# Optimization experiments

Hardware: AMD Instinct MI355X
Metric: run time of the kernel (lower is better)

The kernel has to match this reference:

```python
import jax, jax.numpy as jnp
import numpy as np

TAU = 2.0  # aggregator_temp


def setup_inputs() -> dict:
    key = jax.random.key(0)
    k1, k2 = jax.random.split(key)
    B, Na, Nv, D = 32, 512, 256, 384
    audio_feats = jax.random.normal(k1, (B, Na, D), dtype=jnp.float32)
    visual_feats = jax.random.normal(k2, (B, Nv, D), dtype=jnp.float32)
    return {"audio_feats": audio_feats, "visual_feats": visual_feats}


def reference(audio_feats, visual_feats):
    # Cross-batch token similarities: (B, B, Na, Nv)
    # token_sims[i, j, n, m] = <audio_feats[i, n], visual_feats[j, m]>
    token_sims = jnp.einsum('ind,jmd->ijnm', audio_feats, visual_feats)
    # logsumexp_pool: tau * logsumexp(sims / tau) over key-token dim (Nv),
    # then mean over query-token dim (Na) -> clip_sims (B, B)
    aggregator = TAU * jax.nn.logsumexp(token_sims / TAU, axis=-1)
    clip_sims = aggregator.mean(axis=-1)
    return clip_sims
```

## Files before the change

### kernel.cpp

```cpp
#include <hip/hip_runtime.h>

constexpr int B_  = 32;
constexpr int Na  = 512;
constexpr int Nv  = 256;
constexpr int D   = 384;

constexpr int NK2 = D / 64;

constexpr int AGROUPS = B_ * 16;
constexpr int BGROUPS = B_ * 8;
constexpr size_t GROUP_BYTES = 12 * 1024;
constexpr int SCALE_ONE = 0x7F7F7F7F;

typedef int   int4v    __attribute__((ext_vector_type(4)));
typedef int   int8v    __attribute__((ext_vector_type(8)));
typedef float floatx16 __attribute__((ext_vector_type(16)));

__device__ __forceinline__ void async_load16(const void* g, void* l) {
    __builtin_amdgcn_global_load_lds(
        (const __attribute__((address_space(1))) unsigned int*)g,
        (__attribute__((address_space(3))) unsigned int*)l,
        16, 0, 0);
}

__global__ void convert_fp8_kernel(const float* __restrict__ a, const float* __restrict__ v,
                                   unsigned char* __restrict__ a8,
                                   unsigned char* __restrict__ b8,
                                   float* __restrict__ out) {
    int gid = blockIdx.x * blockDim.x + threadIdx.x;
    if (gid < B_ * B_) out[gid] = 0.0f;

    const int blk = blockIdx.x / 3;
    const int p   = blockIdx.x % 3;
    const bool isA = blk < AGROUPS;
    const float* src;
    unsigned char* dst;
    if (isA) {
        src = a + (size_t)blk * 32 * D;
        dst = a8 + (size_t)blk * GROUP_BYTES;
    } else {
        int b2 = blk - AGROUPS;
        src = v + (size_t)b2 * 32 * D;
        dst = b8 + (size_t)b2 * GROUP_BYTES;
    }
    const int t = threadIdx.x;
    const int r = t >> 3, q = t & 7;

    int k0 = p * 128 + q * 16;
    const float4* s4 = (const float4*)(src + (size_t)r * D + k0);
    float4 f0 = s4[0], f1 = s4[1], f2 = s4[2], f3 = s4[3];
    int w0 = 0, w1 = 0, w2 = 0, w3 = 0;
    w0 = __builtin_amdgcn_cvt_pk_fp8_f32(f0.x, f0.y, w0, false);
    w0 = __builtin_amdgcn_cvt_pk_fp8_f32(f0.z, f0.w, w0, true);
    w1 = __builtin_amdgcn_cvt_pk_fp8_f32(f1.x, f1.y, w1, false);
    w1 = __builtin_amdgcn_cvt_pk_fp8_f32(f1.z, f1.w, w1, true);
    w2 = __builtin_amdgcn_cvt_pk_fp8_f32(f2.x, f2.y, w2, false);
    w2 = __builtin_amdgcn_cvt_pk_fp8_f32(f2.z, f2.w, w2, true);
    w3 = __builtin_amdgcn_cvt_pk_fp8_f32(f3.x, f3.y, w3, false);
    w3 = __builtin_amdgcn_cvt_pk_fp8_f32(f3.z, f3.w, w3, true);
    int kc = k0 >> 5;
    int h2 = (k0 >> 4) & 1;
    size_t off;
    if (isA) {
        off = (size_t)kc * 1024 + h2 * 512 + r * 16;
    } else {
        int q2 = kc >> 1, u = kc & 1, l = r + 32 * h2;
        off = (size_t)q2 * 2048 + l * 32 + u * 16;
    }
    int4v o = { w0, w1, w2, w3 };
    *(int4v*)(dst + off) = o;
}

__device__ __forceinline__ float expsum16(floatx16 a) {
    constexpr float INV_TAU_LN2 = 0.7213475204444817f;
    float e[16];
    #pragma unroll
    for (int i = 0; i < 16; ++i)
        e[i] = __builtin_amdgcn_exp2f(a[i] * INV_TAU_LN2);
    float t0 = (e[0] + e[1])  + (e[2] + e[3]);
    float t1 = (e[4] + e[5])  + (e[6] + e[7]);
    float t2 = (e[8] + e[9])  + (e[10] + e[11]);
    float t3 = (e[12] + e[13]) + (e[14] + e[15]);
    return (t0 + t1) + (t2 + t3);
}

__global__ __launch_bounds__(256, 2) void gemm_lse_kernel(
        const unsigned char* __restrict__ a8,
        const unsigned char* __restrict__ b8,
        float* __restrict__ out)
{
    __shared__ unsigned char ldsA[48 * 1024];
    __shared__ float ms[4][4][32];

    const int tid  = threadIdx.x;
    const int lane = tid & 63;
    const int wn   = tid >> 6;

    int b = blockIdx.x;
    const int xcd   = b & 7;      b >>= 3;
    const int bi_lo = b & 3;      b >>= 2;
    const int rb    = b & 3;      b >>= 2;
    const int bj    = b;
    const int bi    = xcd * 4 + bi_lo;

    {
        const unsigned char* gsrc = a8 + (size_t)(bi * 16 + rb * 4 + wn) * GROUP_BYTES
                                       + (size_t)lane * 16;
        unsigned char* ldst = ldsA + (size_t)wn * GROUP_BYTES;
        #pragma unroll
        for (int kc = 0; kc < 12; ++kc)
            async_load16(gsrc + (size_t)kc * 1024, ldst + kc * 1024);
    }
    __syncthreads();

    const unsigned char* pv0 = b8 + (size_t)(bj * 8 + wn * 2) * GROUP_BYTES
                                  + (size_t)lane * 32;
    const unsigned char* pv1 = pv0 + GROUP_BYTES;
    const unsigned char* la  = ldsA + (size_t)lane * 16;

    floatx16 acc[4][2];
    #pragma unroll
    for (int g = 0; g < 4; ++g)
        #pragma unroll
        for (int vg = 0; vg < 2; ++vg)
            acc[g][vg] = (floatx16)(0.0f);

    int8v Vc0 = *(const int8v*)pv0;
    int8v Vc1 = *(const int8v*)pv1;

    #pragma unroll
    for (int q2 = 0; q2 < NK2; ++q2) {
        int8v Vn0, Vn1;
        if (q2 + 1 < NK2) {
            Vn0 = *(const int8v*)(pv0 + (size_t)(q2 + 1) * 2048);
            Vn1 = *(const int8v*)(pv1 + (size_t)(q2 + 1) * 2048);
        }
        int8v A[4];
        #pragma unroll
        for (int g = 0; g < 4; ++g) {
            const unsigned char* p = la + (size_t)g * GROUP_BYTES + (size_t)q2 * 2048;
            int4v lo = *(const int4v*)p;
            int4v hi = *(const int4v*)(p + 1024);
            A[g] = __builtin_shufflevector(lo, hi, 0, 1, 2, 3, 4, 5, 6, 7);
        }
        __builtin_amdgcn_s_setprio(1);
        #pragma unroll
        for (int g = 0; g < 4; ++g) {
            acc[g][0] = __builtin_amdgcn_mfma_scale_f32_32x32x64_f8f6f4(
                Vc0, A[g], acc[g][0], 0, 0, 0, SCALE_ONE, 0, SCALE_ONE);
            acc[g][1] = __builtin_amdgcn_mfma_scale_f32_32x32x64_f8f6f4(
                Vc1, A[g], acc[g][1], 0, 0, 0, SCALE_ONE, 0, SCALE_ONE);
        }
        __builtin_amdgcn_s_setprio(0);
        if (q2 + 1 < NK2) { Vc0 = Vn0; Vc1 = Vn1; }
    }

    float s[4];
    #pragma unroll
    for (int g = 0; g < 4; ++g) {
        s[g] = expsum16(acc[g][0]) + expsum16(acc[g][1]);
        s[g] += __shfl_xor(s[g], 32);
    }
    if (lane < 32) {
        #pragma unroll
        for (int g = 0; g < 4; ++g)
            ms[wn][g][lane] = s[g];
    }
    __syncthreads();

    if (tid < 128) {
        const int g = tid >> 5, r = tid & 31;
        float e = (ms[0][g][r] + ms[1][g][r]) + (ms[2][g][r] + ms[3][g][r]);
        constexpr float TAU_LN2 = 1.3862943611198906f;
        float lse = TAU_LN2 * __builtin_amdgcn_logf(e);
        #pragma unroll
        for (int m = 1; m < 64; m <<= 1) lse += __shfl_xor(lse, m);
        if ((tid & 63) == 0)
            atomicAdd(&out[bi * 32 + bj], lse * (1.0f / Na));
    }
}

extern "C" void kernel_launch(void* const* d_in, const int* in_sizes, int n_in,
                              void* d_out, int out_size, void* d_ws, size_t ws_size,
                              hipStream_t stream) {
    const float* audio  = (const float*)d_in[0];
    const float* visual = (const float*)d_in[1];
    float* out = (float*)d_out;

    unsigned char* a8 = (unsigned char*)d_ws;
    unsigned char* b8 = a8 + (size_t)AGROUPS * GROUP_BYTES;

    convert_fp8_kernel<<<dim3((AGROUPS + BGROUPS) * 3), dim3(256), 0, stream>>>(
        audio, visual, a8, b8, out);
    gemm_lse_kernel<<<dim3(4096), dim3(256), 0, stream>>>(a8, b8, out);
}
```

Before: 127.0 us.

## Loop each block over eight visual batches to reuse LDS-resident audio tile

```diff
diff --git a/kernel.cpp b/kernel.cpp
--- a/kernel.cpp
+++ b/kernel.cpp
@@ -90,7 +90,7 @@
         float* __restrict__ out)
 {
     __shared__ unsigned char ldsA[48 * 1024];
-    __shared__ float ms[4][4][32];
+    __shared__ float ms[8][4][4][32];
 
     const int tid  = threadIdx.x;
     const int lane = tid & 63;
@@ -100,7 +100,7 @@
     const int xcd   = b & 7;      b >>= 3;
     const int bi_lo = b & 3;      b >>= 2;
     const int rb    = b & 3;      b >>= 2;
-    const int bj    = b;
+    const int bjq   = b;
     const int bi    = xcd * 4 + bi_lo;
 
     {
@@ -113,70 +113,81 @@
     }
     __syncthreads();
 
-    const unsigned char* pv0 = b8 + (size_t)(bj * 8 + wn * 2) * GROUP_BYTES
+    const unsigned char* la = ldsA + (size_t)lane * 16;
+    const unsigned char* pv0 = b8 + (size_t)((bjq * 8) * 8 + wn * 2) * GROUP_BYTES
                                   + (size_t)lane * 32;
-    const unsigned char* pv1 = pv0 + GROUP_BYTES;
-    const unsigned char* la  = ldsA + (size_t)lane * 16;
-
-    floatx16 acc[4][2];
+
+    int8v Vc0 = *(const int8v*)pv0;
+    int8v Vc1 = *(const int8v*)(pv0 + GROUP_BYTES);
+
+    for (int ti = 0; ti < 8; ++ti) {
+        floatx16 acc[4][2];
+        #pragma unroll
+        for (int g = 0; g < 4; ++g)
+            #pragma unroll
+            for (int vg = 0; vg < 2; ++vg)
+                acc[g][vg] = (floatx16)(0.0f);
+
+        #pragma unroll
+        for (int q2 = 0; q2 < NK2; ++q2) {
+            const bool pre = (q2 < NK2 - 1) || (ti < 7);
+            int8v Vn0, Vn1;
+            if (pre) {
+                const unsigned char* np = (q2 < NK2 - 1)
+                    ? pv0 + (size_t)(q2 + 1) * 2048
+                    : pv0 + (size_t)8 * GROUP_BYTES;
+                Vn0 = *(const int8v*)np;
+                Vn1 = *(const int8v*)(np + GROUP_BYTES);
+            }
+            int8v A[4];
+            #pragma unroll
+            for (int g = 0; g < 4; ++g) {
+                const unsigned char* p = la + (size_t)g * GROUP_BYTES + (size_t)q2 * 2048;
+                int4v lo = *(const int4v*)p;
+                int4v hi = *(const int4v*)(p + 1024);
+                A[g] = __builtin_shufflevector(lo, hi, 0, 1, 2, 3, 4, 5, 6, 7);
+            }
+            __builtin_amdgcn_s_setprio(1);
+            #pragma unroll
+            for (int g = 0; g < 4; ++g) {
+                acc[g][0] = __builtin_amdgcn_mfma_scale_f32_32x32x64_f8f6f4(
+                    Vc0, A[g], acc[g][0], 0, 0, 0, SCALE_ONE, 0, SCALE_ONE);
+                acc[g][1] = __builtin_amdgcn_mfma_scale_f32_32x32x64_f8f6f4(
+                    Vc1, A[g], acc[g][1], 0, 0, 0, SCALE_ONE, 0, SCALE_ONE);
+            }
+            __builtin_amdgcn_s_setprio(0);
+            if (pre) { Vc0 = Vn0; Vc1 = Vn1; }
+        }
+        pv0 += (size_t)8 * GROUP_BYTES;
+
+        #pragma unroll
+        for (int g = 0; g < 4; ++g) {
+            float s = expsum16(acc[g][0]) + expsum16(acc[g][1]);
+            s += __shfl_xor(s, 32);
+            if (lane < 32) ms[ti][wn][g][lane] = s;
+        }
+    }
+
+    __syncthreads();
+
     #pragma unroll
-    for (int g = 0; g < 4; ++g)
-        #pragma unroll
-        for (int vg = 0; vg < 2; ++vg)
-            acc[g][vg] = (floatx16)(0.0f);
-
-    int8v Vc0 = *(const int8v*)pv0;
-    int8v Vc1 = *(const int8v*)pv1;
-
-    #pragma unroll
-    for (int q2 = 0; q2 < NK2; ++q2) {
-        int8v Vn0, Vn1;
-        if (q2 + 1 < NK2) {
-            Vn0 = *(const int8v*)(pv0 + (size_t)(q2 + 1) * 2048);
-            Vn1 = *(const int8v*)(pv1 + (size_t)(q2 + 1) * 2048);
+    for (int p2 = 0; p2 < 2; ++p2) {
+        const int ti = wn * 2 + p2;
+        float acc_lse = 0.0f;
+        #pragma unroll
+        for (int pass = 0; pass < 2; ++pass) {
+            const int row = pass * 64 + lane;
+            const int g = row >> 5, r = row & 31;
+            float e = (ms[ti][0][g][r] + ms[ti][1][g][r])
+                    + (ms[ti][2][g][r] + ms[ti][3][g][r]);
+            constexpr float TAU_LN2 = 1.3862943611198906f;
+            float lse = TAU_LN2 * __builtin_amdgcn_logf(e);
+            #pragma unroll
+            for (int m = 1; m < 64; m <<= 1) lse += __shfl_xor(lse, m);
+            acc_lse += lse;
         }
-        int8v A[4];
-        #pragma unroll
-        for (int g = 0; g < 4; ++g) {
-            const unsigned char* p = la + (size_t)g * GROUP_BYTES + (size_t)q2 * 2048;
-            int4v lo = *(const int4v*)p;
-            int4v hi = *(const int4v*)(p + 1024);
-            A[g] = __builtin_shufflevector(lo, hi, 0, 1, 2, 3, 4, 5, 6, 7);
-        }
-        __builtin_amdgcn_s_setprio(1);
-        #pragma unroll
-        for (int g = 0; g < 4; ++g) {
-            acc[g][0] = __builtin_amdgcn_mfma_scale_f32_32x32x64_f8f6f4(
-                Vc0, A[g], acc[g][0], 0, 0, 0, SCALE_ONE, 0, SCALE_ONE);
-            acc[g][1] = __builtin_amdgcn_mfma_scale_f32_32x32x64_f8f6f4(
-                Vc1, A[g], acc[g][1], 0, 0, 0, SCALE_ONE, 0, SCALE_ONE);
-        }
-        __builtin_amdgcn_s_setprio(0);
-        if (q2 + 1 < NK2) { Vc0 = Vn0; Vc1 = Vn1; }
-    }
-
-    float s[4];
-    #pragma unroll
-    for (int g = 0; g < 4; ++g) {
-        s[g] = expsum16(acc[g][0]) + expsum16(acc[g][1]);
-        s[g] += __shfl_xor(s[g], 32);
-    }
-    if (lane < 32) {
-        #pragma unroll
-        for (int g = 0; g < 4; ++g)
-            ms[wn][g][lane] = s[g];
-    }
-    __syncthreads();
-
-    if (tid < 128) {
-        const int g = tid >> 5, r = tid & 31;
-        float e = (ms[0][g][r] + ms[1][g][r]) + (ms[2][g][r] + ms[3][g][r]);
-        constexpr float TAU_LN2 = 1.3862943611198906f;
-        float lse = TAU_LN2 * __builtin_amdgcn_logf(e);
-        #pragma unroll
-        for (int m = 1; m < 64; m <<= 1) lse += __shfl_xor(lse, m);
-        if ((tid & 63) == 0)
-            atomicAdd(&out[bi * 32 + bj], lse * (1.0f / Na));
+        if (lane == 0)
+            atomicAdd(&out[bi * 32 + bjq * 8 + ti], acc_lse * (1.0f / Na));
     }
 }
 
@@ -192,5 +203,5 @@
 
     convert_fp8_kernel<<<dim3((AGROUPS + BGROUPS) * 3), dim3(256), 0, stream>>>(
         audio, visual, a8, b8, out);
-    gemm_lse_kernel<<<dim3(4096), dim3(256), 0, stream>>>(a8, b8, out);
-}
+    gemm_lse_kernel<<<dim3(512), dim3(256), 0, stream>>>(a8, b8, out);
+}
```

New measurement: 150.8 us. 18.7% more time.
